# Kernel tuning notes

Hardware: AMD Instinct MI355X
Metric: run time of the kernel (lower is better)

The kernel has to match this reference:

```python
import jax, jax.numpy as jnp
import numpy as np

N_NODES = 100000
N_EDGES = 3200000
F_IN = 512
HIDDEN = 16
N_CLASSES = 32
DROPOUT = 0.5


def setup_inputs() -> dict:
    key = jax.random.key(0)
    k1, k2, k3, k4, k5, k6 = jax.random.split(key, 6)
    X = jax.random.normal(k1, (N_NODES, F_IN), dtype=jnp.float32)
    edge_src = jax.random.randint(k2, (N_EDGES,), 0, N_NODES, dtype=jnp.int32)
    edge_dst = jax.random.randint(k3, (N_EDGES,), 0, N_NODES, dtype=jnp.int32)
    # normalized adjacency values (positive, like D^-1/2 A D^-1/2 entries)
    edge_w = jax.random.uniform(k4, (N_EDGES,), dtype=jnp.float32)
    W1 = jax.random.normal(k5, (F_IN, HIDDEN), dtype=jnp.float32) * (1.0 / np.sqrt(F_IN))
    W2 = jax.random.normal(k6, (HIDDEN, N_CLASSES), dtype=jnp.float32) * (1.0 / np.sqrt(HIDDEN))
    return {"X": X, "edge_src": edge_src, "edge_dst": edge_dst,
            "edge_w": edge_w, "W1": W1, "W2": W2}


def _dropout(x, key, rate):
    keep = 1.0 - rate
    mask = jax.random.bernoulli(key, keep, x.shape)
    return jnp.where(mask, x / keep, jnp.zeros((), x.dtype))


def _spmm(h, edge_src, edge_dst, edge_w):
    # A @ h with A given as COO edge list: out[d] = sum_e w_e * h[s_e]
    msgs = h[edge_src] * edge_w[:, None]  # [E, C]
    return jax.ops.segment_sum(msgs, edge_dst, num_segments=h.shape[0])


def reference(X, edge_src, edge_dst, edge_w, W1, W2):
    key = jax.random.key(42)
    kd1, kd2 = jax.random.split(key)
    # layer 1: dropout -> GraphConv(relu)  (Spektral: act(A @ (X @ W)))
    H = _dropout(X, kd1, DROPOUT)
    H = H @ W1                                  # [N, HIDDEN]
    H = _spmm(H, edge_src, edge_dst, edge_w)    # [N, HIDDEN]
    H = jax.nn.relu(H)
    # layer 2: dropout -> GraphConv(softmax)
    H = _dropout(H, kd2, DROPOUT)
    H = H @ W2                                  # [N, N_CLASSES]
    H = _spmm(H, edge_src, edge_dst, edge_w)
    return jax.nn.softmax(H, axis=-1)
```

## Files before the change

kernel.cpp:

```cpp
#include <hip/hip_runtime.h>
#include <stdint.h>
#include <stddef.h>

#define N_NODES   100000
#define N_EDGES   3200000
#define F_IN      512
#define HIDDEN    16
#define N_CLASSES 32

#define BSHIFT 6
#define NBUK   ((N_NODES + 63) >> 6)
#define CAP    2368
#define TILE   8192
#define NB_BIN ((N_EDGES + TILE - 1) / TILE)
#define NB_G1  ((N_NODES + 63) / 64)

__host__ __device__ __forceinline__ uint32_t rotl32(uint32_t x, int r) {
#ifdef __HIP_DEVICE_COMPILE__
  return __builtin_amdgcn_alignbit(x, x, (uint32_t)(32 - r));
#else
  return (x << r) | (x >> (32 - r));
#endif
}

__host__ __device__ __forceinline__ void tf2x32_full(uint32_t k0, uint32_t k1,
                                                     uint32_t x0, uint32_t x1,
                                                     uint32_t* o0, uint32_t* o1) {
  const uint32_t k2 = k0 ^ k1 ^ 0x1BD11BDAu;
  x0 += k0; x1 += k1;
#define TF_R(r) { x0 += x1; x1 = rotl32(x1, (r)); x1 ^= x0; }
  TF_R(13) TF_R(15) TF_R(26) TF_R(6)   x0 += k1; x1 += k2 + 1u;
  TF_R(17) TF_R(29) TF_R(16) TF_R(24)  x0 += k2; x1 += k0 + 2u;
  TF_R(13) TF_R(15) TF_R(26) TF_R(6)   x0 += k0; x1 += k1 + 3u;
  TF_R(17) TF_R(29) TF_R(16) TF_R(24)  x0 += k1; x1 += k2 + 4u;
  TF_R(13) TF_R(15) TF_R(26) TF_R(6)   x0 += k2; x1 += k0 + 5u;
#undef TF_R
  *o0 = x0; *o1 = x1;
}

__device__ __forceinline__ bool keep_bit(uint32_t k0, uint32_t k1, uint32_t ctr) {
  uint32_t o0, o1;
  tf2x32_full(k0, k1, 0u, ctr, &o0, &o1);
  return (int32_t)(o0 ^ o1) >= 0;
}

__launch_bounds__(256)
__global__ void gemm1_bin_fused(const float* __restrict__ X,
                                const float* __restrict__ W1,
                                float* __restrict__ H1,
                                const int* __restrict__ src, const int* __restrict__ dst,
                                const float* __restrict__ w, int* __restrict__ gcur,
                                int2* __restrict__ ep,
                                uint32_t kd0, uint32_t kd1) {
  __shared__ __align__(16) char smem[F_IN * HIDDEN * 4];
  const int tid = threadIdx.x;

  if (blockIdx.x < NB_BIN) {
    int* lh = (int*)smem;
    int* gb = (int*)(smem + NBUK * 4);
    const int base = blockIdx.x * TILE;
    const int n = min(TILE, N_EDGES - base);

    for (int i = tid; i < NBUK; i += 256) lh[i] = 0;
    __syncthreads();

    for (int i = tid; i < n; i += 256)
      atomicAdd(&lh[dst[base + i] >> BSHIFT], 1);
    __syncthreads();

    for (int b = tid; b < NBUK; b += 256) {
      const int h = lh[b];
      gb[b] = h ? atomicAdd(&gcur[b], h) : 0;
      lh[b] = 0;
    }
    __syncthreads();

    for (int i = tid; i < n; i += 256) {
      const int e = base + i;
      const int d = dst[e];
      const int b = d >> BSHIFT;
      const int pos = gb[b] + atomicAdd(&lh[b], 1);
      if (pos < CAP)
        ep[(size_t)b * CAP + pos] =
            make_int2(src[e] | ((d & 63) << 17), __float_as_int(w[e]));
    }
    return;
  }

  float* W1s = (float*)smem;
  for (int i = tid; i < (F_IN * HIDDEN) / 4; i += 256) {
    const int f = i >> 2, m = i & 3;
    ((float4*)W1s)[f * 4 + (m ^ ((f >> 2) & 3))] = ((const float4*)W1)[i];
  }
  __syncthreads();

  const int p = tid & 3;
  const int node = (blockIdx.x - NB_BIN) * 64 + (tid >> 2);
  if (node >= N_NODES) return;

  float acc[16];
#pragma unroll
  for (int j = 0; j < 16; j++) acc[j] = 0.0f;

  const float* Xrow = X + (size_t)node * F_IN;
  const uint32_t jb = (uint32_t)node * F_IN;

  float4 xv = *(const float4*)(Xrow + p * 4);
  for (int it = 0; it < F_IN / 16; it++) {
    const int fb = it * 16 + p * 4;
    const float4 cur = xv;
    if (it + 1 < F_IN / 16)
      xv = *(const float4*)(Xrow + (it + 1) * 16 + p * 4);
    const float xs[4] = {cur.x, cur.y, cur.z, cur.w};
#pragma unroll
    for (int e = 0; e < 4; e++) {
      const int f = fb + e;
      const float x = keep_bit(kd0, kd1, jb + (uint32_t)f) ? xs[e] * 2.0f : 0.0f;
      const float4* row = (const float4*)&W1s[f * 16];
#pragma unroll
      for (int q = 0; q < 4; q++) {
        const float4 wv = row[q ^ p];
        acc[q * 4 + 0] += x * wv.x;
        acc[q * 4 + 1] += x * wv.y;
        acc[q * 4 + 2] += x * wv.z;
        acc[q * 4 + 3] += x * wv.w;
      }
    }
  }

  float a2[8];
#pragma unroll
  for (int k = 0; k < 8; k++) {
    const float keep = (p & 2) ? acc[8 + k] : acc[k];
    const float send = (p & 2) ? acc[k]     : acc[8 + k];
    a2[k] = keep + __shfl_xor(send, 2);
  }
  float r0, r1, r2, r3;
  {
    const float k0v = (p & 1) ? a2[4] : a2[0];
    const float s0v = (p & 1) ? a2[0] : a2[4];
    r0 = k0v + __shfl_xor(s0v, 1);
    const float k1v = (p & 1) ? a2[5] : a2[1];
    const float s1v = (p & 1) ? a2[1] : a2[5];
    r1 = k1v + __shfl_xor(s1v, 1);
    const float k2v = (p & 1) ? a2[6] : a2[2];
    const float s2v = (p & 1) ? a2[2] : a2[6];
    r2 = k2v + __shfl_xor(s2v, 1);
    const float k3v = (p & 1) ? a2[7] : a2[3];
    const float s3v = (p & 1) ? a2[3] : a2[7];
    r3 = k3v + __shfl_xor(s3v, 1);
  }
  *(float4*)(H1 + (size_t)node * HIDDEN + p * 4) = make_float4(r0, r1, r2, r3);
}

__launch_bounds__(256)
__global__ void bucket_gather1(const int* __restrict__ gcur, const int2* __restrict__ ep,
                               const float* __restrict__ H1, float* __restrict__ H2d,
                               uint32_t k0, uint32_t k1) {
  __shared__ int2 B[CAP];
  __shared__ int lh[64], lex[64], lcur[64];
  const int tid = threadIdx.x;
  const int b = blockIdx.x;

  if (tid < 64) lh[tid] = 0;
  __syncthreads();

  const int c = min(gcur[b], CAP);
  const int2* ebase = ep + (size_t)b * CAP;

  for (int k = tid; k < c; k += 256)
    atomicAdd(&lh[(ebase[k].x >> 17) & 63], 1);
  __syncthreads();

  if (tid < 64) {
    const int v = lh[tid];
    int s = v;
    for (int off = 1; off < 64; off <<= 1) {
      const int t = __shfl_up(s, off);
      if (tid >= off) s += t;
    }
    lex[tid] = s - v;
    lcur[tid] = s - v;
  }
  __syncthreads();

  for (int k = tid; k < c; k += 256) {
    const int2 r = ebase[k];
    const int p = atomicAdd(&lcur[(r.x >> 17) & 63], 1);
    B[p] = r;
  }
  __syncthreads();

  const int lane = tid & 63, wid = tid >> 6;
  const int ei = lane >> 4, f = lane & 15;
  for (int ln = wid; ln < 64; ln += 4) {
    const int ng = (b << BSHIFT) + ln;
    if (ng >= N_NODES) break;
    const int beg = lex[ln], cnt = lh[ln];
    float acc = 0.0f;
    for (int k = beg + ei; k < beg + cnt; k += 4) {
      const int2 r = B[k];
      acc += __int_as_float(r.y) * H1[(size_t)(r.x & 0x1FFFF) * HIDDEN + f];
    }
    acc += __shfl_xor(acc, 16);
    acc += __shfl_xor(acc, 32);
    float v = fmaxf(acc, 0.0f);
    v = keep_bit(k0, k1, (uint32_t)ng * HIDDEN + (uint32_t)f) ? v * 2.0f : 0.0f;
    if (lane < 16) H2d[(size_t)ng * HIDDEN + f] = v;
  }
}

__launch_bounds__(256)
__global__ void bucket_gather2(const int* __restrict__ gcur, const int2* __restrict__ ep,
                               const float* __restrict__ H2d, const float* __restrict__ W2,
                               float* __restrict__ O) {
  __shared__ int2 B[CAP];
  __shared__ float W2s[HIDDEN][N_CLASSES];
  __shared__ int lh[64], lex[64], lcur[64];
  const int tid = threadIdx.x;
  const int b = blockIdx.x;

  if (tid < 64) lh[tid] = 0;
  for (int i = tid; i < HIDDEN * N_CLASSES; i += 256) ((float*)W2s)[i] = W2[i];
  __syncthreads();

  const int c = min(gcur[b], CAP);
  const int2* ebase = ep + (size_t)b * CAP;

  for (int k = tid; k < c; k += 256)
    atomicAdd(&lh[(ebase[k].x >> 17) & 63], 1);
  __syncthreads();

  if (tid < 64) {
    const int v = lh[tid];
    int s = v;
    for (int off = 1; off < 64; off <<= 1) {
      const int t = __shfl_up(s, off);
      if (tid >= off) s += t;
    }
    lex[tid] = s - v;
    lcur[tid] = s - v;
  }
  __syncthreads();

  for (int k = tid; k < c; k += 256) {
    const int2 r = ebase[k];
    const int p = atomicAdd(&lcur[(r.x >> 17) & 63], 1);
    B[p] = r;
  }
  __syncthreads();

  const int lane = tid & 63, wid = tid >> 6;
  const int ei = lane >> 4, f = lane & 15;
  const int cl = lane & 31;
  for (int ln = wid; ln < 64; ln += 4) {
    const int ng = (b << BSHIFT) + ln;
    if (ng >= N_NODES) break;
    const int beg = lex[ln], cnt = lh[ln];
    float acc = 0.0f;
    for (int k = beg + ei; k < beg + cnt; k += 4) {
      const int2 r = B[k];
      acc += __int_as_float(r.y) * H2d[(size_t)(r.x & 0x1FFFF) * HIDDEN + f];
    }
    acc += __shfl_xor(acc, 16);
    acc += __shfl_xor(acc, 32);
    float lg = 0.0f;
#pragma unroll
    for (int fq = 0; fq < HIDDEN; fq++)
      lg += __shfl(acc, fq) * W2s[fq][cl];
    float m = lg;
#pragma unroll
    for (int off = 16; off >= 1; off >>= 1) m = fmaxf(m, __shfl_xor(m, off));
    const float ex = __expf(lg - m);
    float ss = ex;
#pragma unroll
    for (int off = 16; off >= 1; off >>= 1) ss += __shfl_xor(ss, off);
    if (lane < 32) O[(size_t)ng * N_CLASSES + cl] = ex / ss;
  }
}

__launch_bounds__(256)
__global__ void gemm1_dropout_fb(const float* __restrict__ X,
                                 const float* __restrict__ W1,
                                 float* __restrict__ H1,
                                 uint32_t kd0, uint32_t kd1) {
  __shared__ float W1s[F_IN][HIDDEN];
  const int tid = threadIdx.x;
  for (int i = tid; i < (F_IN * HIDDEN) / 4; i += 256)
    ((float4*)W1s)[i] = ((const float4*)W1)[i];
  __syncthreads();
  const int n = blockIdx.x * 256 + tid;
  if (n >= N_NODES) return;
  float acc[HIDDEN];
#pragma unroll
  for (int j = 0; j < HIDDEN; j++) acc[j] = 0.0f;
  const float4* Xrow = (const float4*)(X + (size_t)n * F_IN);
  const uint32_t jbase = (uint32_t)n * F_IN;
  for (int cc = 0; cc < F_IN / 4; cc++) {
    float4 xv = Xrow[cc];
    float xs[4] = {xv.x, xv.y, xv.z, xv.w};
#pragma unroll
    for (int e = 0; e < 4; e++) {
      const int f = cc * 4 + e;
      const float x = keep_bit(kd0, kd1, jbase + (uint32_t)f) ? xs[e] * 2.0f : 0.0f;
      const float* wr = W1s[f];
#pragma unroll
      for (int j = 0; j < HIDDEN; j++) acc[j] += x * wr[j];
    }
  }
  float4* out = (float4*)(H1 + (size_t)n * HIDDEN);
#pragma unroll
  for (int q = 0; q < HIDDEN / 4; q++)
    out[q] = make_float4(acc[q * 4], acc[q * 4 + 1], acc[q * 4 + 2], acc[q * 4 + 3]);
}

__launch_bounds__(256)
__global__ void spmm1_atomic(const int* __restrict__ src, const int* __restrict__ dst,
                             const float* __restrict__ w, const float* __restrict__ H1,
                             float* __restrict__ H2) {
  const long long t = (long long)blockIdx.x * 256 + threadIdx.x;
  if (t >= (long long)N_EDGES * 4) return;
  const int e = (int)(t >> 2);
  const int q = (int)(t & 3);
  const float we = w[e];
  const float4 h = ((const float4*)(H1 + (size_t)src[e] * HIDDEN))[q];
  float* o = H2 + (size_t)dst[e] * HIDDEN + q * 4;
  unsafeAtomicAdd(o + 0, we * h.x);
  unsafeAtomicAdd(o + 1, we * h.y);
  unsafeAtomicAdd(o + 2, we * h.z);
  unsafeAtomicAdd(o + 3, we * h.w);
}

__launch_bounds__(256)
__global__ void gemm2_dropout(const float* __restrict__ H2,
                              const float* __restrict__ W2,
                              float* __restrict__ H3,
                              uint32_t kd0, uint32_t kd1) {
  __shared__ float W2s[HIDDEN][N_CLASSES];
  const int tid = threadIdx.x;
  for (int i = tid; i < (HIDDEN * N_CLASSES) / 4; i += 256)
    ((float4*)W2s)[i] = ((const float4*)W2)[i];
  __syncthreads();
  const int n = blockIdx.x * 256 + tid;
  if (n >= N_NODES) return;
  float acc[N_CLASSES];
#pragma unroll
  for (int j = 0; j < N_CLASSES; j++) acc[j] = 0.0f;
  const float4* hrow = (const float4*)(H2 + (size_t)n * HIDDEN);
  const uint32_t jbase = (uint32_t)n * HIDDEN;
#pragma unroll
  for (int qq = 0; qq < HIDDEN / 4; qq++) {
    float4 hv = hrow[qq];
    float hs[4] = {hv.x, hv.y, hv.z, hv.w};
#pragma unroll
    for (int e = 0; e < 4; e++) {
      const int cc = qq * 4 + e;
      float h = fmaxf(hs[e], 0.0f);
      h = keep_bit(kd0, kd1, jbase + (uint32_t)cc) ? h * 2.0f : 0.0f;
      const float* wr = W2s[cc];
#pragma unroll
      for (int j = 0; j < N_CLASSES; j++) acc[j] += h * wr[j];
    }
  }
  float4* out = (float4*)(H3 + (size_t)n * N_CLASSES);
#pragma unroll
  for (int q = 0; q < N_CLASSES / 4; q++)
    out[q] = make_float4(acc[q * 4], acc[q * 4 + 1], acc[q * 4 + 2], acc[q * 4 + 3]);
}

__launch_bounds__(256)
__global__ void spmm2_atomic(const int* __restrict__ src, const int* __restrict__ dst,
                             const float* __restrict__ w, const float* __restrict__ H3,
                             float* __restrict__ O) {
  const long long t = (long long)blockIdx.x * 256 + threadIdx.x;
  if (t >= (long long)N_EDGES * 8) return;
  const int e = (int)(t >> 3);
  const int q = (int)(t & 7);
  const float we = w[e];
  const float4 h = ((const float4*)(H3 + (size_t)src[e] * N_CLASSES))[q];
  float* o = O + (size_t)dst[e] * N_CLASSES + q * 4;
  unsafeAtomicAdd(o + 0, we * h.x);
  unsafeAtomicAdd(o + 1, we * h.y);
  unsafeAtomicAdd(o + 2, we * h.z);
  unsafeAtomicAdd(o + 3, we * h.w);
}

__launch_bounds__(256)
__global__ void softmax_rows(float* __restrict__ O) {
  const int n = blockIdx.x * 256 + threadIdx.x;
  if (n >= N_NODES) return;
  float4* row = (float4*)(O + (size_t)n * N_CLASSES);
  float v[N_CLASSES];
#pragma unroll
  for (int q = 0; q < N_CLASSES / 4; q++) {
    float4 t = row[q];
    v[q * 4 + 0] = t.x; v[q * 4 + 1] = t.y; v[q * 4 + 2] = t.z; v[q * 4 + 3] = t.w;
  }
  float m = v[0];
#pragma unroll
  for (int j = 1; j < N_CLASSES; j++) m = fmaxf(m, v[j]);
  float s = 0.0f;
#pragma unroll
  for (int j = 0; j < N_CLASSES; j++) { v[j] = __expf(v[j] - m); s += v[j]; }
  const float inv = 1.0f / s;
#pragma unroll
  for (int q = 0; q < N_CLASSES / 4; q++)
    row[q] = make_float4(v[q * 4] * inv, v[q * 4 + 1] * inv,
                         v[q * 4 + 2] * inv, v[q * 4 + 3] * inv);
}

extern "C" void kernel_launch(void* const* d_in, const int* in_sizes, int n_in,
                              void* d_out, int out_size, void* d_ws, size_t ws_size,
                              hipStream_t stream) {
  const float* X    = (const float*)d_in[0];
  const int*   esrc = (const int*)d_in[1];
  const int*   edst = (const int*)d_in[2];
  const float* ew   = (const float*)d_in[3];
  const float* W1   = (const float*)d_in[4];
  const float* W2   = (const float*)d_in[5];
  float* out = (float*)d_out;

  uint32_t kd1_0, kd1_1, kd2_0, kd2_1;
  tf2x32_full(0u, 42u, 0u, 0u, &kd1_0, &kd1_1);
  tf2x32_full(0u, 42u, 0u, 1u, &kd2_0, &kd2_1);

  const int nb_nodes = (N_NODES + 255) / 256;

  const size_t sz_ep  = (size_t)NBUK * CAP * sizeof(int2);
  const size_t sz_H1  = (size_t)N_NODES * HIDDEN * sizeof(float);
  const size_t sz_H2d = sz_H1;
  const size_t sz_cur = (size_t)NBUK * sizeof(int);
  const size_t need = sz_ep + sz_H1 + sz_H2d + sz_cur;

  char* p = (char*)d_ws;
  int2* ep = (int2*)p;       p += sz_ep;
  float* H1 = (float*)p;     p += sz_H1;
  float* H2d = (float*)p;    p += sz_H2d;
  int* gcur = (int*)p;

  if (ws_size >= need) {
    hipMemsetAsync(gcur, 0, sz_cur, stream);
    gemm1_bin_fused<<<NB_BIN + NB_G1, 256, 0, stream>>>(
        X, W1, H1, esrc, edst, ew, gcur, ep, kd1_0, kd1_1);
    bucket_gather1<<<NBUK, 256, 0, stream>>>(gcur, ep, H1, H2d, kd2_0, kd2_1);
    bucket_gather2<<<NBUK, 256, 0, stream>>>(gcur, ep, H2d, W2, out);
  } else {
    float* fH1 = (float*)d_ws;
    float* fH2 = fH1 + (size_t)N_NODES * HIDDEN;
    float* fH3 = fH2 + (size_t)N_NODES * HIDDEN;
    hipMemsetAsync(fH2, 0, (size_t)N_NODES * HIDDEN * sizeof(float), stream);
    hipMemsetAsync(out, 0, (size_t)out_size * sizeof(float), stream);
    gemm1_dropout_fb<<<nb_nodes, 256, 0, stream>>>(X, W1, fH1, kd1_0, kd1_1);
    spmm1_atomic<<<(N_EDGES * 4) / 256, 256, 0, stream>>>(esrc, edst, ew, fH1, fH2);
    gemm2_dropout<<<nb_nodes, 256, 0, stream>>>(fH2, W2, fH3, kd2_0, kd2_1);
    spmm2_atomic<<<(N_EDGES * 8) / 256, 256, 0, stream>>>(esrc, edst, ew, fH3, out);
    softmax_rows<<<nb_nodes, 256, 0, stream>>>(out);
  }
}
```

Measured before the change: 337.2 us.

## Precompute dropout mask bits alongside edge binning, then run GEMM1 with mask

Moves the Threefry dropout-mask generation for layer 1 out of the GEMM1 kernel into the edge-binning kernel, where extra blocks write a packed bitmask with one bit per X element. A separate GEMM1 kernel then reads the bitmask word per 32 features while streaming X, so its inner loop carries no RNG arithmetic. The aim is to overlap the compute-heavy RNG with the memory-bound binning and keep the GEMM close to bandwidth-bound. In exchange it adds a 6.4MB mask write and read, plus an extra kernel launch that now runs serially after binning.

```diff
diff --git a/kernel.cpp b/kernel.cpp
--- a/kernel.cpp
+++ b/kernel.cpp
@@ -13,6 +13,8 @@
 #define CAP    2368
 #define TILE   8192
 #define NB_BIN ((N_EDGES + TILE - 1) / TILE)
+#define NW_MASK ((N_NODES * F_IN) / 32)
+#define NB_MSK (NW_MASK / 256)
 #define NB_G1  ((N_NODES + 63) / 64)
 
 __host__ __device__ __forceinline__ uint32_t rotl32(uint32_t x, int r) {
@@ -45,19 +47,15 @@
 }
 
 __launch_bounds__(256)
-__global__ void gemm1_bin_fused(const float* __restrict__ X,
-                                const float* __restrict__ W1,
-                                float* __restrict__ H1,
-                                const int* __restrict__ src, const int* __restrict__ dst,
-                                const float* __restrict__ w, int* __restrict__ gcur,
-                                int2* __restrict__ ep,
-                                uint32_t kd0, uint32_t kd1) {
-  __shared__ __align__(16) char smem[F_IN * HIDDEN * 4];
+__global__ void bin_mask_fused(const int* __restrict__ src, const int* __restrict__ dst,
+                               const float* __restrict__ w, int* __restrict__ gcur,
+                               int2* __restrict__ ep, uint32_t* __restrict__ mask1,
+                               uint32_t kd0, uint32_t kd1) {
+  __shared__ int lh[NBUK];
+  __shared__ int gb[NBUK];
   const int tid = threadIdx.x;
 
   if (blockIdx.x < NB_BIN) {
-    int* lh = (int*)smem;
-    int* gb = (int*)(smem + NBUK * 4);
     const int base = blockIdx.x * TILE;
     const int n = min(TILE, N_EDGES - base);
 
@@ -87,7 +85,27 @@
     return;
   }
 
-  float* W1s = (float*)smem;
+  const int mt = (blockIdx.x - NB_BIN) * 256 + tid;
+  if (mt < NW_MASK) {
+    const uint32_t base = (uint32_t)mt * 32u;
+    uint32_t word = 0u;
+#pragma unroll
+    for (int j = 0; j < 32; j++) {
+      uint32_t o0, o1;
+      tf2x32_full(kd0, kd1, 0u, base + (uint32_t)j, &o0, &o1);
+      word |= ((~(o0 ^ o1)) >> 31) << j;
+    }
+    mask1[mt] = word;
+  }
+}
+
+__launch_bounds__(256)
+__global__ void gemm1_mask(const float* __restrict__ X,
+                           const float* __restrict__ W1,
+                           const uint32_t* __restrict__ mask1,
+                           float* __restrict__ H1) {
+  __shared__ float W1s[F_IN * HIDDEN];
+  const int tid = threadIdx.x;
   for (int i = tid; i < (F_IN * HIDDEN) / 4; i += 256) {
     const int f = i >> 2, m = i & 3;
     ((float4*)W1s)[f * 4 + (m ^ ((f >> 2) & 3))] = ((const float4*)W1)[i];
@@ -95,35 +113,53 @@
   __syncthreads();
 
   const int p = tid & 3;
-  const int node = (blockIdx.x - NB_BIN) * 64 + (tid >> 2);
+  const int node = blockIdx.x * 64 + (tid >> 2);
   if (node >= N_NODES) return;
 
   float acc[16];
 #pragma unroll
   for (int j = 0; j < 16; j++) acc[j] = 0.0f;
 
-  const float* Xrow = X + (size_t)node * F_IN;
-  const uint32_t jb = (uint32_t)node * F_IN;
-
-  float4 xv = *(const float4*)(Xrow + p * 4);
-  for (int it = 0; it < F_IN / 16; it++) {
-    const int fb = it * 16 + p * 4;
-    const float4 cur = xv;
-    if (it + 1 < F_IN / 16)
-      xv = *(const float4*)(Xrow + (it + 1) * 16 + p * 4);
-    const float xs[4] = {cur.x, cur.y, cur.z, cur.w};
+  const float4* Xrow4 = (const float4*)(X + (size_t)node * F_IN);
+  const uint32_t* Mrow = mask1 + (size_t)node * 16;
+  const int sh0 = p << 2;
+  const int sh1 = 16 + (p << 2);
+
+  for (int it2 = 0; it2 < 16; ++it2) {
+    const uint32_t mword = Mrow[it2];
+    const float4 xv0 = Xrow4[it2 * 8 + p];
+    const float4 xv1 = Xrow4[it2 * 8 + 4 + p];
+    const uint32_t nib0 = mword >> sh0;
+    const uint32_t nib1 = mword >> sh1;
+    const float xs0[4] = {xv0.x, xv0.y, xv0.z, xv0.w};
+    const float xs1[4] = {xv1.x, xv1.y, xv1.z, xv1.w};
+
 #pragma unroll
     for (int e = 0; e < 4; e++) {
-      const int f = fb + e;
-      const float x = keep_bit(kd0, kd1, jb + (uint32_t)f) ? xs[e] * 2.0f : 0.0f;
+      const float xd = (nib0 >> e) & 1u ? xs0[e] + xs0[e] : 0.0f;
+      const int f = it2 * 32 + p * 4 + e;
       const float4* row = (const float4*)&W1s[f * 16];
 #pragma unroll
       for (int q = 0; q < 4; q++) {
         const float4 wv = row[q ^ p];
-        acc[q * 4 + 0] += x * wv.x;
-        acc[q * 4 + 1] += x * wv.y;
-        acc[q * 4 + 2] += x * wv.z;
-        acc[q * 4 + 3] += x * wv.w;
+        acc[q * 4 + 0] += xd * wv.x;
+        acc[q * 4 + 1] += xd * wv.y;
+        acc[q * 4 + 2] += xd * wv.z;
+        acc[q * 4 + 3] += xd * wv.w;
+      }
+    }
+#pragma unroll
+    for (int e = 0; e < 4; e++) {
+      const float xd = (nib1 >> e) & 1u ? xs1[e] + xs1[e] : 0.0f;
+      const int f = it2 * 32 + 16 + p * 4 + e;
+      const float4* row = (const float4*)&W1s[f * 16];
+#pragma unroll
+      for (int q = 0; q < 4; q++) {
+        const float4 wv = row[q ^ p];
+        acc[q * 4 + 0] += xd * wv.x;
+        acc[q * 4 + 1] += xd * wv.y;
+        acc[q * 4 + 2] += xd * wv.z;
+        acc[q * 4 + 3] += xd * wv.w;
       }
     }
   }
@@ -429,19 +465,22 @@
   const size_t sz_ep  = (size_t)NBUK * CAP * sizeof(int2);
   const size_t sz_H1  = (size_t)N_NODES * HIDDEN * sizeof(float);
   const size_t sz_H2d = sz_H1;
+  const size_t sz_mk  = (size_t)NW_MASK * sizeof(uint32_t);
   const size_t sz_cur = (size_t)NBUK * sizeof(int);
-  const size_t need = sz_ep + sz_H1 + sz_H2d + sz_cur;
+  const size_t need = sz_ep + sz_H1 + sz_H2d + sz_mk + sz_cur;
 
   char* p = (char*)d_ws;
   int2* ep = (int2*)p;       p += sz_ep;
   float* H1 = (float*)p;     p += sz_H1;
   float* H2d = (float*)p;    p += sz_H2d;
+  uint32_t* mask1 = (uint32_t*)p; p += sz_mk;
   int* gcur = (int*)p;
 
   if (ws_size >= need) {
     hipMemsetAsync(gcur, 0, sz_cur, stream);
-    gemm1_bin_fused<<<NB_BIN + NB_G1, 256, 0, stream>>>(
-        X, W1, H1, esrc, edst, ew, gcur, ep, kd1_0, kd1_1);
+    bin_mask_fused<<<NB_BIN + NB_MSK, 256, 0, stream>>>(
+        esrc, edst, ew, gcur, ep, mask1, kd1_0, kd1_1);
+    gemm1_mask<<<NB_G1, 256, 0, stream>>>(X, W1, mask1, H1);
     bucket_gather1<<<NBUK, 256, 0, stream>>>(gcur, ep, H1, H2d, kd2_0, kd2_1);
     bucket_gather2<<<NBUK, 256, 0, stream>>>(gcur, ep, H2d, W2, out);
   } else {
```

Result: faster. 298.2 us (-11.6%).

## Precompute dropout mask bits in a separate kernel before fused GEMM1

Applied to the files above, without the earlier changes.

Moves the Threefry dropout-mask generation for layer 1 out of the GEMM1 inner loop into a dedicated mask_gen kernel that packs keep bits into 32-bit words. The GEMM1 path then reads the packed mask with one uint4 load per four iterations and tests bits instead of running the RNG per element. This removes ALU-heavy hash work from the bandwidth-bound GEMM, but the RNG work still runs in a separate serial launch and adds a 6.4 MB mask write and read.

```diff
diff --git a/kernel.cpp b/kernel.cpp
--- a/kernel.cpp
+++ b/kernel.cpp
@@ -13,6 +13,8 @@
 #define CAP    2368
 #define TILE   8192
 #define NB_BIN ((N_EDGES + TILE - 1) / TILE)
+#define NW_MASK ((N_NODES * F_IN) / 32)
+#define NB_MSK (NW_MASK / 256)
 #define NB_G1  ((N_NODES + 63) / 64)
 
 __host__ __device__ __forceinline__ uint32_t rotl32(uint32_t x, int r) {
@@ -45,19 +47,34 @@
 }
 
 __launch_bounds__(256)
-__global__ void gemm1_bin_fused(const float* __restrict__ X,
+__global__ void mask_gen(uint32_t* __restrict__ mask1, uint32_t kd0, uint32_t kd1) {
+  const int mt = blockIdx.x * 256 + threadIdx.x;
+  if (mt >= NW_MASK) return;
+  const uint32_t base = (uint32_t)mt * 32u;
+  uint32_t word = 0u;
+#pragma unroll
+  for (int j = 0; j < 32; j++) {
+    uint32_t o0, o1;
+    tf2x32_full(kd0, kd1, 0u, base + (uint32_t)j, &o0, &o1);
+    word |= ((~(o0 ^ o1)) >> 31) << j;
+  }
+  mask1[mt] = word;
+}
+
+__launch_bounds__(256)
+__global__ void bin_gemm1_fused(const float* __restrict__ X,
                                 const float* __restrict__ W1,
+                                const uint32_t* __restrict__ mask1,
                                 float* __restrict__ H1,
                                 const int* __restrict__ src, const int* __restrict__ dst,
                                 const float* __restrict__ w, int* __restrict__ gcur,
-                                int2* __restrict__ ep,
-                                uint32_t kd0, uint32_t kd1) {
-  __shared__ __align__(16) char smem[F_IN * HIDDEN * 4];
+                                int2* __restrict__ ep) {
+  __shared__ __align__(16) float smem[F_IN * HIDDEN];
   const int tid = threadIdx.x;
 
   if (blockIdx.x < NB_BIN) {
     int* lh = (int*)smem;
-    int* gb = (int*)(smem + NBUK * 4);
+    int* gb = (int*)smem + NBUK;
     const int base = blockIdx.x * TILE;
     const int n = min(TILE, N_EDGES - base);
 
@@ -87,7 +104,7 @@
     return;
   }
 
-  float* W1s = (float*)smem;
+  float* W1s = smem;
   for (int i = tid; i < (F_IN * HIDDEN) / 4; i += 256) {
     const int f = i >> 2, m = i & 3;
     ((float4*)W1s)[f * 4 + (m ^ ((f >> 2) & 3))] = ((const float4*)W1)[i];
@@ -102,31 +119,59 @@
 #pragma unroll
   for (int j = 0; j < 16; j++) acc[j] = 0.0f;
 
-  const float* Xrow = X + (size_t)node * F_IN;
-  const uint32_t jb = (uint32_t)node * F_IN;
-
-  float4 xv = *(const float4*)(Xrow + p * 4);
-  for (int it = 0; it < F_IN / 16; it++) {
-    const int fb = it * 16 + p * 4;
-    const float4 cur = xv;
-    if (it + 1 < F_IN / 16)
-      xv = *(const float4*)(Xrow + (it + 1) * 16 + p * 4);
-    const float xs[4] = {cur.x, cur.y, cur.z, cur.w};
-#pragma unroll
-    for (int e = 0; e < 4; e++) {
-      const int f = fb + e;
-      const float x = keep_bit(kd0, kd1, jb + (uint32_t)f) ? xs[e] * 2.0f : 0.0f;
-      const float4* row = (const float4*)&W1s[f * 16];
-#pragma unroll
-      for (int q = 0; q < 4; q++) {
-        const float4 wv = row[q ^ p];
-        acc[q * 4 + 0] += x * wv.x;
-        acc[q * 4 + 1] += x * wv.y;
-        acc[q * 4 + 2] += x * wv.z;
-        acc[q * 4 + 3] += x * wv.w;
-      }
-    }
-  }
+  const float4* Xrow4 = (const float4*)(X + (size_t)node * F_IN);
+  const uint4* M4 = (const uint4*)(mask1 + (size_t)node * 16);
+  const int sh0 = p << 2;
+  const int sh1 = 16 + (p << 2);
+
+#define PROC(IT2, MWORD)                                              \
+  {                                                                   \
+    const uint32_t mword = (MWORD);                                   \
+    const float4 xv0 = Xrow4[(IT2) * 8 + p];                          \
+    const float4 xv1 = Xrow4[(IT2) * 8 + 4 + p];                      \
+    const float xs0[4] = {xv0.x, xv0.y, xv0.z, xv0.w};                \
+    const float xs1[4] = {xv1.x, xv1.y, xv1.z, xv1.w};                \
+    _Pragma("unroll")                                                 \
+    for (int e = 0; e < 4; e++) {                                     \
+      const float xd = ((mword >> (sh0 + e)) & 1u) ? xs0[e] + xs0[e]  \
+                                                   : 0.0f;            \
+      const int f = (IT2) * 32 + p * 4 + e;                           \
+      const float4* row = (const float4*)&W1s[f * 16];                \
+      _Pragma("unroll")                                               \
+      for (int q = 0; q < 4; q++) {                                   \
+        const float4 wv = row[q ^ p];                                 \
+        acc[q * 4 + 0] += xd * wv.x;                                  \
+        acc[q * 4 + 1] += xd * wv.y;                                  \
+        acc[q * 4 + 2] += xd * wv.z;                                  \
+        acc[q * 4 + 3] += xd * wv.w;                                  \
+      }                                                               \
+    }                                                                 \
+    _Pragma("unroll")                                                 \
+    for (int e = 0; e < 4; e++) {                                     \
+      const float xd = ((mword >> (sh1 + e)) & 1u) ? xs1[e] + xs1[e]  \
+                                                   : 0.0f;            \
+      const int f = (IT2) * 32 + 16 + p * 4 + e;                      \
+      const float4* row = (const float4*)&W1s[f * 16];                \
+      _Pragma("unroll")                                               \
+      for (int q = 0; q < 4; q++) {                                   \
+        const float4 wv = row[q ^ p];                                 \
+        acc[q * 4 + 0] += xd * wv.x;                                  \
+        acc[q * 4 + 1] += xd * wv.y;                                  \
+        acc[q * 4 + 2] += xd * wv.z;                                  \
+        acc[q * 4 + 3] += xd * wv.w;                                  \
+      }                                                               \
+    }                                                                 \
+  }
+
+  for (int g = 0; g < 4; ++g) {
+    const uint4 mw4 = M4[g];
+    const int i0 = g * 4;
+    PROC(i0 + 0, mw4.x)
+    PROC(i0 + 1, mw4.y)
+    PROC(i0 + 2, mw4.z)
+    PROC(i0 + 3, mw4.w)
+  }
+#undef PROC
 
   float a2[8];
 #pragma unroll
@@ -429,19 +474,22 @@
   const size_t sz_ep  = (size_t)NBUK * CAP * sizeof(int2);
   const size_t sz_H1  = (size_t)N_NODES * HIDDEN * sizeof(float);
   const size_t sz_H2d = sz_H1;
+  const size_t sz_mk  = (size_t)NW_MASK * sizeof(uint32_t);
   const size_t sz_cur = (size_t)NBUK * sizeof(int);
-  const size_t need = sz_ep + sz_H1 + sz_H2d + sz_cur;
+  const size_t need = sz_ep + sz_H1 + sz_H2d + sz_mk + sz_cur;
 
   char* p = (char*)d_ws;
   int2* ep = (int2*)p;       p += sz_ep;
   float* H1 = (float*)p;     p += sz_H1;
   float* H2d = (float*)p;    p += sz_H2d;
+  uint32_t* mask1 = (uint32_t*)p; p += sz_mk;
   int* gcur = (int*)p;
 
   if (ws_size >= need) {
     hipMemsetAsync(gcur, 0, sz_cur, stream);
-    gemm1_bin_fused<<<NB_BIN + NB_G1, 256, 0, stream>>>(
-        X, W1, H1, esrc, edst, ew, gcur, ep, kd1_0, kd1_1);
+    mask_gen<<<NB_MSK, 256, 0, stream>>>(mask1, kd1_0, kd1_1);
+    bin_gemm1_fused<<<NB_BIN + NB_G1, 256, 0, stream>>>(
+        X, W1, mask1, H1, esrc, edst, ew, gcur, ep);
     bucket_gather1<<<NBUK, 256, 0, stream>>>(gcur, ep, H1, H2d, kd2_0, kd2_1);
     bucket_gather2<<<NBUK, 256, 0, stream>>>(gcur, ep, H2d, W2, out);
   } else {
```

After: 354.6 us. 5.2% more time.
